# Kernel optimization log

Measured on AMD Instinct MI355X. Metric: run time of the kernel, lower is better.

## Reference

```python
import jax, jax.numpy as jnp
import numpy as np

START_ID = 1  # id of the start symbol in the vocabulary


def setup_inputs() -> dict:
    key = jax.random.key(0)
    ks = jax.random.split(key, 11)
    B, T, V, E, H, F = 64, 32, 10000, 300, 256, 4096
    s = 0.05
    return {
        "X": jax.random.normal(ks[0], (B, F), jnp.float32),
        "emb_table": jax.random.normal(ks[1], (V, E), jnp.float32),
        "fc1_w": jax.random.normal(ks[2], (H, F), jnp.float32) * s,
        "fc1_b": jax.random.normal(ks[3], (H,), jnp.float32) * s,
        "w_ih": jax.random.normal(ks[4], (4 * H, H + E), jnp.float32) * s,
        "w_hh": jax.random.normal(ks[5], (4 * H, H), jnp.float32) * s,
        "b_ih": jax.random.normal(ks[6], (4 * H,), jnp.float32) * s,
        "b_hh": jax.random.normal(ks[7], (4 * H,), jnp.float32) * s,
        "fc2_w": jax.random.normal(ks[8], (V, H), jnp.float32) * s,
        "fc2_b": jax.random.normal(ks[9], (V,), jnp.float32) * s,
        "label": jax.random.randint(ks[10], (T, B), 0, V, jnp.int64),
        "max_sentence_len": T,
    }


def reference(X, emb_table, fc1_w, fc1_b, w_ih, w_hh, b_ih, b_hh, fc2_w, fc2_b,
              label, max_sentence_len):
    T = max_sentence_len
    B = X.shape[0]
    V, H = fc2_w.shape
    E = emb_table.shape[1]

    # fc1: project image features to hidden size
    Xp = X @ fc1_w.T + fc1_b  # [B, H]

    # word embedding input per step: step 1 uses start symbol,
    # step idx>=2 uses teacher-forced embedding of label[idx-1]
    start_emb = jnp.broadcast_to(emb_table[START_ID], (1, B, E))
    tf_emb = emb_table[label[1:T - 1]]          # [T-2, B, E]
    embeds = jnp.concatenate([start_emb, tf_emb], axis=0)  # [T-1, B, E]

    h0 = jnp.zeros((B, H), X.dtype)
    c0 = jnp.zeros((B, H), X.dtype)

    def step(carry, e):
        h, c = carry
        x = jnp.concatenate([Xp, e], axis=1)  # [B, H+E]
        gates = x @ w_ih.T + b_ih + h @ w_hh.T + b_hh  # [B, 4H]
        i, f, g, o = jnp.split(gates, 4, axis=1)
        i = jax.nn.sigmoid(i)
        f = jax.nn.sigmoid(f)
        g = jnp.tanh(g)
        o = jax.nn.sigmoid(o)
        c = f * c + i * g
        h = o * jnp.tanh(c)
        logp = jax.nn.log_softmax(h @ fc2_w.T + fc2_b, axis=-1)  # [B, V]
        return (h, c), logp

    _, probs = jax.lax.scan(step, (h0, c0), embeds)  # [T-1, B, V]

    # first timestep: one-hot of the start word (as in the torch code)
    start_onehot = jnp.zeros((1, B, V), X.dtype).at[:, :, START_ID].set(1.0)
    result = jnp.concatenate([start_onehot, probs], axis=0)  # [T, B, V]
    return jnp.transpose(result, (1, 0, 2))  # [B, T, V]
```

## Files before the change

### kernel.cpp

```cpp
#include <hip/hip_runtime.h>
#include <hip/hip_bf16.h>
#include <math.h>

#define B_   64
#define T_   32
#define S_   31
#define V_   10000
#define E_   300
#define H_   256
#define F_   4096
#define G4   1024
#define HE   556
#define MPAD 2048
#define NPAD 10112
#define START_ID 1
#define NBL  4

#define FP0 10112
#define FP1 (FP0 + 128)
#define FP2 (FP1 + 2500)
#define FP3 (FP2 + 512)
#define FP4 (FP3 + 300)

typedef __bf16 bf16x8 __attribute__((ext_vector_type(8)));
typedef float  f32x4  __attribute__((ext_vector_type(4)));

__device__ __forceinline__ float bf16bits_to_f(unsigned int u) {
    union { unsigned int i; float f; } c; c.i = u; return c.f;
}
__device__ __forceinline__ unsigned short f_to_bf16bits(float f) {
    union { float f; unsigned int i; } c; c.f = f;
    unsigned int r = c.i + 0x7fffu + ((c.i >> 16) & 1);
    return (unsigned short)(r >> 16);
}
__device__ __forceinline__ float sigm(float x) { return 1.f / (1.f + __expf(-x)); }
__device__ __forceinline__ float tanh_fast(float x) { return 1.f - 2.f / (__expf(2.f * x) + 1.f); }

__device__ __forceinline__ void pina(bf16x8 &v) {
    union { bf16x8 b; unsigned int u[4]; } x;
    x.b = v;
    asm volatile("" : "+a"(x.u[0]), "+a"(x.u[1]), "+a"(x.u[2]), "+a"(x.u[3]));
    v = x.b;
}

__global__ void k_front(const float* __restrict__ fc2_w,
                        __hip_bfloat16* __restrict__ fc2bf,
                        __hip_bfloat16* __restrict__ Hs,
                        const float* __restrict__ w_hh,
                        unsigned short* __restrict__ wpack,
                        float* __restrict__ out,
                        const float* __restrict__ X,
                        const float* __restrict__ fc1_w,
                        const float* __restrict__ fc1_b,
                        float* __restrict__ Xp_part,
                        const float* __restrict__ w_ih,
                        float* __restrict__ wie) {
    int bid = blockIdx.x, tid = threadIdx.x;
    if (bid < FP0) {
        size_t i = (size_t)bid * 256 + tid;
        float v = (i < (size_t)V_ * H_) ? fc2_w[i] : 0.f;
        fc2bf[i] = __float2bfloat16(v);
        if (i < (size_t)(MPAD - S_ * B_) * H_)
            Hs[(size_t)S_ * B_ * H_ + i] = __float2bfloat16(0.f);
    } else if (bid < FP1) {
        int t = (bid - FP0) * 256 + tid;
        int lane = t & 63, frag = t >> 6;
        int kf = frag & 7, nt = (frag >> 3) & 7, w = frag >> 6;
        int l16 = lane & 15, quad = lane >> 4;
        int j = (l16 & 3) * 256 + w * 32 + nt * 4 + (l16 >> 2);
        int k0 = kf * 32 + quad * 8;
        const float* src = w_hh + (size_t)j * H_ + k0;
        float4 a0 = *(const float4*)(src);
        float4 a1 = *(const float4*)(src + 4);
        unsigned short pk[8];
        pk[0] = f_to_bf16bits(a0.x); pk[1] = f_to_bf16bits(a0.y);
        pk[2] = f_to_bf16bits(a0.z); pk[3] = f_to_bf16bits(a0.w);
        pk[4] = f_to_bf16bits(a1.x); pk[5] = f_to_bf16bits(a1.y);
        pk[6] = f_to_bf16bits(a1.z); pk[7] = f_to_bf16bits(a1.w);
        uint4 st;
        st.x = (unsigned)pk[0] | ((unsigned)pk[1] << 16);
        st.y = (unsigned)pk[2] | ((unsigned)pk[3] << 16);
        st.z = (unsigned)pk[4] | ((unsigned)pk[5] << 16);
        st.w = (unsigned)pk[6] | ((unsigned)pk[7] << 16);
        *(uint4*)(wpack + (size_t)frag * 512 + lane * 8) = st;
    } else if (bid < FP2) {
        int i = (bid - FP1) * 256 + tid;
        if (i < B_ * V_) {
            int b = i / V_, v = i - b * V_;
            out[(size_t)b * T_ * V_ + v] = (v == START_ID) ? 1.f : 0.f;
        }
    } else if (bid < FP3) {
        __shared__ __align__(16) float xs[512];
        int r = bid - FP2;
        int b = r >> 3, q = r & 7;
        const float4* xrow = (const float4*)(X + (size_t)b * F_ + q * 512);
        if (tid < 128) ((float4*)xs)[tid] = xrow[tid];
        __syncthreads();
        int k = tid;
        const float4* w = (const float4*)(fc1_w + (size_t)k * F_ + q * 512);
        float acc = 0.f;
        #pragma unroll 8
        for (int f = 0; f < 128; ++f) {
            float4 wv = w[f];
            float4 xv = ((const float4*)xs)[f];
            acc += wv.x * xv.x + wv.y * xv.y + wv.z * xv.z + wv.w * xv.w;
        }
        if (q == 0) acc += fc1_b[k];
        Xp_part[((size_t)(q * 64 + b)) * 256 + k] = acc;
    } else if (bid < FP4) {
        int idx = (bid - FP3) * 256 + tid;
        int kk = idx >> 10, j = idx & 1023;
        float4 v = *(const float4*)(w_ih + (size_t)j * HE + H_ + kk * 4);
        ((float4*)wie)[(size_t)kk * 1024 + j] = v;
    }
}

__global__ void k_gconst(const float* __restrict__ Xp_part, const float* __restrict__ w_ih,
                         const float* __restrict__ b_ih, const float* __restrict__ b_hh,
                         float* __restrict__ gconst) {
    __shared__ __align__(16) float xs[H_];
    int b = blockIdx.x;
    float s = 0.f;
    #pragma unroll
    for (int q = 0; q < 8; ++q) s += Xp_part[((size_t)(q * 64 + b)) * 256 + threadIdx.x];
    xs[threadIdx.x] = s;
    __syncthreads();
    #pragma unroll
    for (int q = 0; q < 4; ++q) {
        int j = threadIdx.x + q * 256;
        const float* w = w_ih + (size_t)j * HE;
        float acc = 0.f;
        #pragma unroll 8
        for (int k = 0; k < H_ / 4; ++k) {
            float4 wv = *(const float4*)(w + k * 4);
            float4 xv = ((const float4*)xs)[k];
            acc += wv.x * xv.x + wv.y * xv.y + wv.z * xv.z + wv.w * xv.w;
        }
        gconst[b * G4 + j] = acc + b_ih[j] + b_hh[j];
    }
}

__global__ void k_ge(const float* __restrict__ emb, const int* __restrict__ label,
                     const float* __restrict__ wie, const float* __restrict__ gconst,
                     unsigned short* __restrict__ gfullT) {
    __shared__ __align__(16) float es[8][E_];
    int jt = blockIdx.x, bt = blockIdx.y, t = blockIdx.z;
    for (int i = threadIdx.x; i < 8 * E_; i += 256) {
        int b8 = i / E_, e = i - b8 * E_;
        int b = bt * 8 + b8;
        int idx = (t == 0) ? START_ID : label[t * B_ + b];
        es[b8][e] = emb[(size_t)idx * E_ + e];
    }
    __syncthreads();
    int j = jt * 256 + threadIdx.x;
    const float4* wp4 = (const float4*)wie + j;
    float acc[8] = {0.f, 0.f, 0.f, 0.f, 0.f, 0.f, 0.f, 0.f};
    for (int kk = 0; kk < E_ / 4; ++kk) {
        float4 wv = wp4[(size_t)kk * 1024];
        #pragma unroll
        for (int b8 = 0; b8 < 8; ++b8) {
            float4 ev = *(const float4*)(&es[b8][kk * 4]);
            acc[b8] += wv.x * ev.x + wv.y * ev.y + wv.z * ev.z + wv.w * ev.w;
        }
    }
    int u = threadIdx.x;
    int tile = u >> 2;
    int m = (u & 3) * 4 + jt;
    size_t base = ((((size_t)t * NBL + (bt >> 1)) * 64 + tile) * 16 + (bt & 1) * 8) * 16 + m;
    #pragma unroll
    for (int b8 = 0; b8 < 8; ++b8)
        gfullT[base + (size_t)b8 * 16] =
            f_to_bf16bits(acc[b8] + gconst[(bt * 8 + b8) * G4 + j]);
}

__global__ __launch_bounds__(512)
__attribute__((amdgpu_waves_per_eu(2, 2)))
void k_lstm(const unsigned short* __restrict__ gfullT,
            const unsigned short* __restrict__ wpack,
            __hip_bfloat16* __restrict__ Hs_) {
    unsigned short* Hs = (unsigned short*)Hs_;
    int bg = blockIdx.x;
    int tid = threadIdx.x;
    int w = tid >> 6, lane = tid & 63;
    int l16 = lane & 15, quad = lane >> 4;

    __shared__ __align__(16) unsigned short hs0[16 * 264];
    __shared__ __align__(16) unsigned short hs1[16 * 264];
    __shared__ __align__(16) unsigned short blds[8 * 16 * 64 * 8];

    const unsigned short* wpb = wpack + (size_t)(w * 8) * 8 * 512 + lane * 8;

    bf16x8 wr0[8], wr1[8], wr2[8], wr3[8];
    #pragma unroll
    for (int kf = 0; kf < 8; ++kf) {
        wr0[kf] = *(const bf16x8*)(wpb + (0 * 8 + kf) * 512);
        wr1[kf] = *(const bf16x8*)(wpb + (1 * 8 + kf) * 512);
        wr2[kf] = *(const bf16x8*)(wpb + (2 * 8 + kf) * 512);
        wr3[kf] = *(const bf16x8*)(wpb + (3 * 8 + kf) * 512);
    }
    #pragma unroll
    for (int kf = 0; kf < 8; ++kf) {
        pina(wr0[kf]); pina(wr1[kf]); pina(wr2[kf]); pina(wr3[kf]);
    }

    #pragma unroll
    for (int f2 = 0; f2 < 16; ++f2) {
        int nt = 4 + (f2 >> 3), kf = f2 & 7;
        bf16x8 v = *(const bf16x8*)(wpb + (nt * 8 + kf) * 512);
        *(bf16x8*)(blds + ((size_t)(w * 16 + f2) * 64 + lane) * 8) = v;
    }

    for (int i = tid; i < 16 * 264 / 8; i += 512)
        ((uint4*)hs0)[i] = make_uint4(0, 0, 0, 0);
    __syncthreads();

    float c[8] = {0.f, 0.f, 0.f, 0.f, 0.f, 0.f, 0.f, 0.f};
    const unsigned short* bl = blds + (size_t)(w * 16) * 512 + lane * 8;
    int orow = tid >> 5, ocol = tid & 31;

    for (int t = 0; t < S_; ++t) {
        unsigned short* hcur = (t & 1) ? hs1 : hs0;
        unsigned short* hnxt = (t & 1) ? hs0 : hs1;

        const unsigned short* hb = hcur + l16 * 264 + quad * 8;
        bf16x8 hf[8];
        #pragma unroll
        for (int kf = 0; kf < 8; ++kf) hf[kf] = *(const bf16x8*)(hb + kf * 32);

        if (t > 0) {
            uint4 wv = *(const uint4*)(hcur + orow * 264 + ocol * 8);
            *(uint4*)(Hs + ((size_t)((t - 1) * B_ + bg * 16 + orow)) * H_ + ocol * 8) = wv;
        }
        uint2 gf[8];
        const unsigned short* gtb = gfullT +
            ((((size_t)t * NBL + bg) * 64 + w * 8) * 256) + l16 * 16 + quad * 4;
        #pragma unroll
        for (int nt = 0; nt < 8; ++nt) gf[nt] = *(const uint2*)(gtb + nt * 256);
        bf16x8 s6[8];
        #pragma unroll
        for (int kf = 0; kf < 8; ++kf) s6[kf] = *(const bf16x8*)(wpb + (6 * 8 + kf) * 512);

#define DO_NT(nt, WSRC)                                                          \
        {                                                                        \
            f32x4 acc0 = {0.f, 0.f, 0.f, 0.f}, acc1 = {0.f, 0.f, 0.f, 0.f};      \
            _Pragma("unroll")                                                    \
            for (int kf = 0; kf < 8; kf += 2) {                                  \
                acc0 = __builtin_amdgcn_mfma_f32_16x16x32_bf16(WSRC[kf], hf[kf], \
                                                               acc0, 0, 0, 0);  \
                acc1 = __builtin_amdgcn_mfma_f32_16x16x32_bf16(WSRC[kf + 1],     \
                                                               hf[kf + 1],      \
                                                               acc1, 0, 0, 0);  \
            }                                                                    \
            float g0 = acc0[0] + acc1[0] + bf16bits_to_f(gf[nt].x << 16);        \
            float g1 = acc0[1] + acc1[1] + bf16bits_to_f(gf[nt].x & 0xffff0000u);\
            float g2 = acc0[2] + acc1[2] + bf16bits_to_f(gf[nt].y << 16);        \
            float g3 = acc0[3] + acc1[3] + bf16bits_to_f(gf[nt].y & 0xffff0000u);\
            float ig = sigm(g0);                                                 \
            float fg = sigm(g1);                                                 \
            float gg = tanh_fast(g2);                                            \
            float og = sigm(g3);                                                 \
            c[nt] = fg * c[nt] + ig * gg;                                        \
            float hv = og * tanh_fast(c[nt]);                                    \
            hnxt[l16 * 264 + w * 32 + (nt) * 4 + quad] = f_to_bf16bits(hv);      \
        }

        DO_NT(0, wr0)
        DO_NT(1, wr1)
        DO_NT(2, wr2)
        DO_NT(3, wr3)
        {
            bf16x8 w4[8];
            #pragma unroll
            for (int kf = 0; kf < 8; ++kf) w4[kf] = *(const bf16x8*)(bl + kf * 512);
            DO_NT(4, w4)
        }
        bf16x8 s7[8];
        #pragma unroll
        for (int kf = 0; kf < 8; ++kf) s7[kf] = *(const bf16x8*)(wpb + (7 * 8 + kf) * 512);
        {
            bf16x8 w5[8];
            #pragma unroll
            for (int kf = 0; kf < 8; ++kf) w5[kf] = *(const bf16x8*)(bl + (8 + kf) * 512);
            DO_NT(5, w5)
        }
        DO_NT(6, s6)
        DO_NT(7, s7)
#undef DO_NT
        __syncthreads();
    }
    {
        uint4 v = *(const uint4*)(hs1 + orow * 264 + ocol * 8);
        *(uint4*)(Hs + ((size_t)((S_ - 1) * B_ + bg * 16 + orow)) * H_ + ocol * 8) = v;
    }
}

__global__ __launch_bounds__(256) void k_gemm(const unsigned short* __restrict__ A,
                                              const unsigned short* __restrict__ Bw,
                                              const float* __restrict__ bias,
                                              float* __restrict__ out) {
    int nt = blockIdx.x, mt = blockIdx.y;
    int w = threadIdx.x >> 6, lane = threadIdx.x & 63;
    int l16 = lane & 15, quad = lane >> 4;
    int m0 = mt * 128 + (w >> 1) * 64;
    int n0 = nt * 128 + (w & 1) * 64;
    f32x4 acc[4][4] = {};
    const unsigned short* Ap = A + (size_t)(m0 + l16) * H_ + quad * 8;
    const unsigned short* Bp = Bw + (size_t)(n0 + l16) * H_ + quad * 8;
    #pragma unroll
    for (int k = 0; k < H_; k += 32) {
        bf16x8 a[4], bb[4];
        #pragma unroll
        for (int i = 0; i < 4; ++i) {
            a[i]  = *(const bf16x8*)(Ap + (size_t)i * 16 * H_ + k);
            bb[i] = *(const bf16x8*)(Bp + (size_t)i * 16 * H_ + k);
        }
        #pragma unroll
        for (int i = 0; i < 4; ++i)
            #pragma unroll
            for (int jn = 0; jn < 4; ++jn)
                acc[i][jn] = __builtin_amdgcn_mfma_f32_16x16x32_bf16(a[i], bb[jn], acc[i][jn], 0, 0, 0);
    }
    #pragma unroll
    for (int i = 0; i < 4; ++i) {
        #pragma unroll
        for (int jn = 0; jn < 4; ++jn) {
            #pragma unroll
            for (int r = 0; r < 4; ++r) {
                int m = m0 + i * 16 + quad * 4 + r;
                int n = n0 + jn * 16 + l16;
                if (m < S_ * B_ && n < V_) {
                    int t = m >> 6, b = m & 63;
                    out[((size_t)b * T_ + t + 1) * V_ + n] = acc[i][jn][r] + bias[n];
                }
            }
        }
    }
}

__global__ __launch_bounds__(256) void k_lsm(float* __restrict__ out) {
    __shared__ __align__(16) float rowbuf[V_];
    __shared__ float rmx[256], rsum[256];
    int m = blockIdx.x;
    int t = m >> 6, b = m & 63;
    float* row = out + ((size_t)b * T_ + t + 1) * V_;
    int tid = threadIdx.x;
    float mx = -1e30f, sum = 0.f;
    for (int v4 = tid; v4 < V_ / 4; v4 += 256) {
        float4 x = ((const float4*)row)[v4];
        ((float4*)rowbuf)[v4] = x;
        float m4 = fmaxf(fmaxf(x.x, x.y), fmaxf(x.z, x.w));
        if (m4 > mx) { sum *= __expf(mx - m4); mx = m4; }
        sum += __expf(x.x - mx) + __expf(x.y - mx) + __expf(x.z - mx) + __expf(x.w - mx);
    }
    rmx[tid] = mx; rsum[tid] = sum;
    __syncthreads();
    for (int s = 128; s > 0; s >>= 1) {
        if (tid < s) {
            float ma = rmx[tid], mb = rmx[tid + s];
            float sa = rsum[tid], sb = rsum[tid + s];
            float mm = fmaxf(ma, mb);
            rmx[tid] = mm;
            rsum[tid] = sa * __expf(ma - mm) + sb * __expf(mb - mm);
        }
        __syncthreads();
    }
    float lse = rmx[0] + logf(rsum[0]);
    for (int v4 = tid; v4 < V_ / 4; v4 += 256) {
        float4 x = ((const float4*)rowbuf)[v4];
        x.x -= lse; x.y -= lse; x.z -= lse; x.w -= lse;
        ((float4*)row)[v4] = x;
    }
}

extern "C" void kernel_launch(void* const* d_in, const int* in_sizes, int n_in,
                              void* d_out, int out_size, void* d_ws, size_t ws_size,
                              hipStream_t stream) {
    const float* X      = (const float*)d_in[0];
    const float* emb    = (const float*)d_in[1];
    const float* fc1_w  = (const float*)d_in[2];
    const float* fc1_b  = (const float*)d_in[3];
    const float* w_ih   = (const float*)d_in[4];
    const float* w_hh   = (const float*)d_in[5];
    const float* b_ih   = (const float*)d_in[6];
    const float* b_hh   = (const float*)d_in[7];
    const float* fc2_w  = (const float*)d_in[8];
    const float* fc2_b  = (const float*)d_in[9];
    const int*   label  = (const int*)d_in[10];
    float* out = (float*)d_out;

    char* ws = (char*)d_ws;
    float*          Xp_part = (float*)(ws);
    float*          gconst  = (float*)(ws + 524288);
    unsigned short* gfullT  = (unsigned short*)(ws + 786432);
    __hip_bfloat16* Hs      = (__hip_bfloat16*)(ws + 4849664);
    __hip_bfloat16* fc2bf   = (__hip_bfloat16*)(ws + 5898240);
    unsigned short* wpack   = (unsigned short*)(ws + 11075584);
    float*          wie     = (float*)(ws + 11599872);

    k_front <<<FP4, 256, 0, stream>>>(fc2_w, fc2bf, Hs, w_hh, wpack, out,
                                      X, fc1_w, fc1_b, Xp_part, w_ih, wie);
    k_gconst<<<B_, 256, 0, stream>>>(Xp_part, w_ih, b_ih, b_hh, gconst);
    k_ge    <<<dim3(4, 8, S_), 256, 0, stream>>>(emb, label, wie, gconst, gfullT);
    k_lstm  <<<NBL, 512, 0, stream>>>(gfullT, wpack, Hs);
    k_gemm  <<<dim3(NPAD / 128, MPAD / 128), 256, 0, stream>>>((const unsigned short*)Hs,
                                                              (const unsigned short*)fc2bf, fc2_b, out);
    k_lsm   <<<S_ * B_, 256, 0, stream>>>(out);
}
```

Baseline: 503.3 us.

## Fuse LSTM recurrence and fc2 GEMM into one kernel with progress flags

Merges the LSTM recurrence kernel and the output-projection GEMM into a single launch. Four blocks run the recurrence and publish per-timestep progress counters with release atomics. The remaining 252 blocks loop over 256x128 GEMM tiles, spin-waiting with acquire loads until the hidden states their tile needs are written. This lets the projection overlap the serial recurrence instead of waiting for it to finish. It also drops the AGPR pinning and waves_per_eu hint, and seeds the MFMA accumulator with the gate preactivation in a single chain instead of two partial accumulators. The risks are that the spin-waiting blocks compete with the LSTM blocks for resources, and that the longer single MFMA dependency chain adds latency to each recurrence step.

```diff
diff --git a/kernel.cpp b/kernel.cpp
--- a/kernel.cpp
+++ b/kernel.cpp
@@ -15,6 +15,8 @@
 #define NPAD 10112
 #define START_ID 1
 #define NBL  4
+#define NW   252
+#define NTIL (8 * 79)
 
 #define FP0 10112
 #define FP1 (FP0 + 128)
@@ -35,13 +37,6 @@
 }
 __device__ __forceinline__ float sigm(float x) { return 1.f / (1.f + __expf(-x)); }
 __device__ __forceinline__ float tanh_fast(float x) { return 1.f - 2.f / (__expf(2.f * x) + 1.f); }
-
-__device__ __forceinline__ void pina(bf16x8 &v) {
-    union { bf16x8 b; unsigned int u[4]; } x;
-    x.b = v;
-    asm volatile("" : "+a"(x.u[0]), "+a"(x.u[1]), "+a"(x.u[2]), "+a"(x.u[3]));
-    v = x.b;
-}
 
 __global__ void k_front(const float* __restrict__ fc2_w,
                         __hip_bfloat16* __restrict__ fc2bf,
@@ -54,7 +49,8 @@
                         const float* __restrict__ fc1_b,
                         float* __restrict__ Xp_part,
                         const float* __restrict__ w_ih,
-                        float* __restrict__ wie) {
+                        float* __restrict__ wie,
+                        unsigned int* __restrict__ prog) {
     int bid = blockIdx.x, tid = threadIdx.x;
     if (bid < FP0) {
         size_t i = (size_t)bid * 256 + tid;
@@ -62,6 +58,7 @@
         fc2bf[i] = __float2bfloat16(v);
         if (i < (size_t)(MPAD - S_ * B_) * H_)
             Hs[(size_t)S_ * B_ * H_ + i] = __float2bfloat16(0.f);
+        if (bid == 0 && tid < 32) prog[tid] = 0u;
     } else if (bid < FP1) {
         int t = (bid - FP0) * 256 + tid;
         int lane = t & 63, frag = t >> 6;
@@ -174,12 +171,14 @@
 }
 
 __global__ __launch_bounds__(512)
-__attribute__((amdgpu_waves_per_eu(2, 2)))
-void k_lstm(const unsigned short* __restrict__ gfullT,
+void k_back(const unsigned short* __restrict__ gfullT,
             const unsigned short* __restrict__ wpack,
-            __hip_bfloat16* __restrict__ Hs_) {
+            __hip_bfloat16* __restrict__ Hs_,
+            const unsigned short* __restrict__ fc2bf,
+            const float* __restrict__ fc2_b,
+            float* __restrict__ out,
+            unsigned int* __restrict__ prog) {
     unsigned short* Hs = (unsigned short*)Hs_;
-    int bg = blockIdx.x;
     int tid = threadIdx.x;
     int w = tid >> 6, lane = tid & 63;
     int l16 = lane & 15, quad = lane >> 4;
@@ -188,149 +187,155 @@
     __shared__ __align__(16) unsigned short hs1[16 * 264];
     __shared__ __align__(16) unsigned short blds[8 * 16 * 64 * 8];
 
-    const unsigned short* wpb = wpack + (size_t)(w * 8) * 8 * 512 + lane * 8;
-
-    bf16x8 wr0[8], wr1[8], wr2[8], wr3[8];
-    #pragma unroll
-    for (int kf = 0; kf < 8; ++kf) {
-        wr0[kf] = *(const bf16x8*)(wpb + (0 * 8 + kf) * 512);
-        wr1[kf] = *(const bf16x8*)(wpb + (1 * 8 + kf) * 512);
-        wr2[kf] = *(const bf16x8*)(wpb + (2 * 8 + kf) * 512);
-        wr3[kf] = *(const bf16x8*)(wpb + (3 * 8 + kf) * 512);
-    }
-    #pragma unroll
-    for (int kf = 0; kf < 8; ++kf) {
-        pina(wr0[kf]); pina(wr1[kf]); pina(wr2[kf]); pina(wr3[kf]);
-    }
-
-    #pragma unroll
-    for (int f2 = 0; f2 < 16; ++f2) {
-        int nt = 4 + (f2 >> 3), kf = f2 & 7;
-        bf16x8 v = *(const bf16x8*)(wpb + (nt * 8 + kf) * 512);
-        *(bf16x8*)(blds + ((size_t)(w * 16 + f2) * 64 + lane) * 8) = v;
-    }
-
-    for (int i = tid; i < 16 * 264 / 8; i += 512)
-        ((uint4*)hs0)[i] = make_uint4(0, 0, 0, 0);
-    __syncthreads();
-
-    float c[8] = {0.f, 0.f, 0.f, 0.f, 0.f, 0.f, 0.f, 0.f};
-    const unsigned short* bl = blds + (size_t)(w * 16) * 512 + lane * 8;
-    int orow = tid >> 5, ocol = tid & 31;
-
-    for (int t = 0; t < S_; ++t) {
-        unsigned short* hcur = (t & 1) ? hs1 : hs0;
-        unsigned short* hnxt = (t & 1) ? hs0 : hs1;
-
-        const unsigned short* hb = hcur + l16 * 264 + quad * 8;
-        bf16x8 hf[8];
+    if (blockIdx.x < NBL) {
+        int bg = blockIdx.x;
+        const unsigned short* wpb = wpack + (size_t)(w * 8) * 8 * 512 + lane * 8;
+
+        bf16x8 wr0[8], wr1[8], wr2[8], wr3[8];
         #pragma unroll
-        for (int kf = 0; kf < 8; ++kf) hf[kf] = *(const bf16x8*)(hb + kf * 32);
-
-        if (t > 0) {
-            uint4 wv = *(const uint4*)(hcur + orow * 264 + ocol * 8);
-            *(uint4*)(Hs + ((size_t)((t - 1) * B_ + bg * 16 + orow)) * H_ + ocol * 8) = wv;
-        }
-        uint2 gf[8];
-        const unsigned short* gtb = gfullT +
-            ((((size_t)t * NBL + bg) * 64 + w * 8) * 256) + l16 * 16 + quad * 4;
+        for (int kf = 0; kf < 8; ++kf) {
+            wr0[kf] = *(const bf16x8*)(wpb + (0 * 8 + kf) * 512);
+            wr1[kf] = *(const bf16x8*)(wpb + (1 * 8 + kf) * 512);
+            wr2[kf] = *(const bf16x8*)(wpb + (2 * 8 + kf) * 512);
+            wr3[kf] = *(const bf16x8*)(wpb + (3 * 8 + kf) * 512);
+        }
         #pragma unroll
-        for (int nt = 0; nt < 8; ++nt) gf[nt] = *(const uint2*)(gtb + nt * 256);
-        bf16x8 s6[8];
-        #pragma unroll
-        for (int kf = 0; kf < 8; ++kf) s6[kf] = *(const bf16x8*)(wpb + (6 * 8 + kf) * 512);
-
-#define DO_NT(nt, WSRC)                                                          \
-        {                                                                        \
-            f32x4 acc0 = {0.f, 0.f, 0.f, 0.f}, acc1 = {0.f, 0.f, 0.f, 0.f};      \
-            _Pragma("unroll")                                                    \
-            for (int kf = 0; kf < 8; kf += 2) {                                  \
-                acc0 = __builtin_amdgcn_mfma_f32_16x16x32_bf16(WSRC[kf], hf[kf], \
-                                                               acc0, 0, 0, 0);  \
-                acc1 = __builtin_amdgcn_mfma_f32_16x16x32_bf16(WSRC[kf + 1],     \
-                                                               hf[kf + 1],      \
-                                                               acc1, 0, 0, 0);  \
-            }                                                                    \
-            float g0 = acc0[0] + acc1[0] + bf16bits_to_f(gf[nt].x << 16);        \
-            float g1 = acc0[1] + acc1[1] + bf16bits_to_f(gf[nt].x & 0xffff0000u);\
-            float g2 = acc0[2] + acc1[2] + bf16bits_to_f(gf[nt].y << 16);        \
-            float g3 = acc0[3] + acc1[3] + bf16bits_to_f(gf[nt].y & 0xffff0000u);\
-            float ig = sigm(g0);                                                 \
-            float fg = sigm(g1);                                                 \
-            float gg = tanh_fast(g2);                                            \
-            float og = sigm(g3);                                                 \
-            c[nt] = fg * c[nt] + ig * gg;                                        \
-            float hv = og * tanh_fast(c[nt]);                                    \
-            hnxt[l16 * 264 + w * 32 + (nt) * 4 + quad] = f_to_bf16bits(hv);      \
-        }
-
-        DO_NT(0, wr0)
-        DO_NT(1, wr1)
-        DO_NT(2, wr2)
-        DO_NT(3, wr3)
+        for (int f2 = 0; f2 < 16; ++f2) {
+            int nt = 4 + (f2 >> 3), kf = f2 & 7;
+            bf16x8 v = *(const bf16x8*)(wpb + (nt * 8 + kf) * 512);
+            *(bf16x8*)(blds + ((size_t)(w * 16 + f2) * 64 + lane) * 8) = v;
+        }
+        for (int i = tid; i < 16 * 264 / 8; i += 512)
+            ((uint4*)hs0)[i] = make_uint4(0, 0, 0, 0);
+        __syncthreads();
+
+        float c[8] = {0.f, 0.f, 0.f, 0.f, 0.f, 0.f, 0.f, 0.f};
+        const unsigned short* bl = blds + (size_t)(w * 16) * 512 + lane * 8;
+        int orow = tid >> 5, ocol = tid & 31;
+
+        for (int t = 0; t < S_; ++t) {
+            unsigned short* hcur = (t & 1) ? hs1 : hs0;
+            unsigned short* hnxt = (t & 1) ? hs0 : hs1;
+
+            const unsigned short* hb = hcur + l16 * 264 + quad * 8;
+            bf16x8 hf[8];
+            #pragma unroll
+            for (int kf = 0; kf < 8; ++kf) hf[kf] = *(const bf16x8*)(hb + kf * 32);
+
+            if (t > 0) {
+                uint4 wv = *(const uint4*)(hcur + orow * 264 + ocol * 8);
+                *(uint4*)(Hs + ((size_t)((t - 1) * B_ + bg * 16 + orow)) * H_ + ocol * 8) = wv;
+            }
+            uint2 gf[8];
+            const unsigned short* gtb = gfullT +
+                ((((size_t)t * NBL + bg) * 64 + w * 8) * 256) + l16 * 16 + quad * 4;
+            #pragma unroll
+            for (int nt = 0; nt < 8; ++nt) gf[nt] = *(const uint2*)(gtb + nt * 256);
+            bf16x8 s6[8];
+            #pragma unroll
+            for (int kf = 0; kf < 8; ++kf) s6[kf] = *(const bf16x8*)(wpb + (6 * 8 + kf) * 512);
+
+#define DO_NT(nt, WSRC)                                                         \
+            {                                                                   \
+                f32x4 acc;                                                      \
+                acc[0] = bf16bits_to_f(gf[nt].x << 16);                         \
+                acc[1] = bf16bits_to_f(gf[nt].x & 0xffff0000u);                 \
+                acc[2] = bf16bits_to_f(gf[nt].y << 16);                         \
+                acc[3] = bf16bits_to_f(gf[nt].y & 0xffff0000u);                 \
+                _Pragma("unroll")                                               \
+                for (int kf = 0; kf < 8; ++kf)                                  \
+                    acc = __builtin_amdgcn_mfma_f32_16x16x32_bf16(WSRC[kf],     \
+                                                  hf[kf], acc, 0, 0, 0);       \
+                float ig = sigm(acc[0]);                                        \
+                float fg = sigm(acc[1]);                                        \
+                float gg = tanh_fast(acc[2]);                                   \
+                float og = sigm(acc[3]);                                        \
+                c[nt] = fg * c[nt] + ig * gg;                                   \
+                float hv = og * tanh_fast(c[nt]);                               \
+                hnxt[l16 * 264 + w * 32 + (nt) * 4 + quad] = f_to_bf16bits(hv); \
+            }
+
+            DO_NT(0, wr0)
+            DO_NT(1, wr1)
+            DO_NT(2, wr2)
+            DO_NT(3, wr3)
+            {
+                bf16x8 w4[8];
+                #pragma unroll
+                for (int kf = 0; kf < 8; ++kf) w4[kf] = *(const bf16x8*)(bl + kf * 512);
+                DO_NT(4, w4)
+            }
+            bf16x8 s7[8];
+            #pragma unroll
+            for (int kf = 0; kf < 8; ++kf) s7[kf] = *(const bf16x8*)(wpb + (7 * 8 + kf) * 512);
+            {
+                bf16x8 w5[8];
+                #pragma unroll
+                for (int kf = 0; kf < 8; ++kf) w5[kf] = *(const bf16x8*)(bl + (8 + kf) * 512);
+                DO_NT(5, w5)
+            }
+            DO_NT(6, s6)
+            DO_NT(7, s7)
+#undef DO_NT
+            __syncthreads();
+            if (tid == 0 && t > 0)
+                __hip_atomic_fetch_add(&prog[t - 1], 1u, __ATOMIC_RELEASE,
+                                       __HIP_MEMORY_SCOPE_AGENT);
+        }
         {
-            bf16x8 w4[8];
-            #pragma unroll
-            for (int kf = 0; kf < 8; ++kf) w4[kf] = *(const bf16x8*)(bl + kf * 512);
-            DO_NT(4, w4)
-        }
-        bf16x8 s7[8];
-        #pragma unroll
-        for (int kf = 0; kf < 8; ++kf) s7[kf] = *(const bf16x8*)(wpb + (7 * 8 + kf) * 512);
-        {
-            bf16x8 w5[8];
-            #pragma unroll
-            for (int kf = 0; kf < 8; ++kf) w5[kf] = *(const bf16x8*)(bl + (8 + kf) * 512);
-            DO_NT(5, w5)
-        }
-        DO_NT(6, s6)
-        DO_NT(7, s7)
-#undef DO_NT
+            uint4 v = *(const uint4*)(hs1 + orow * 264 + ocol * 8);
+            *(uint4*)(Hs + ((size_t)((S_ - 1) * B_ + bg * 16 + orow)) * H_ + ocol * 8) = v;
+        }
         __syncthreads();
-    }
-    {
-        uint4 v = *(const uint4*)(hs1 + orow * 264 + ocol * 8);
-        *(uint4*)(Hs + ((size_t)((S_ - 1) * B_ + bg * 16 + orow)) * H_ + ocol * 8) = v;
-    }
-}
-
-__global__ __launch_bounds__(256) void k_gemm(const unsigned short* __restrict__ A,
-                                              const unsigned short* __restrict__ Bw,
-                                              const float* __restrict__ bias,
-                                              float* __restrict__ out) {
-    int nt = blockIdx.x, mt = blockIdx.y;
-    int w = threadIdx.x >> 6, lane = threadIdx.x & 63;
-    int l16 = lane & 15, quad = lane >> 4;
-    int m0 = mt * 128 + (w >> 1) * 64;
-    int n0 = nt * 128 + (w & 1) * 64;
-    f32x4 acc[4][4] = {};
-    const unsigned short* Ap = A + (size_t)(m0 + l16) * H_ + quad * 8;
-    const unsigned short* Bp = Bw + (size_t)(n0 + l16) * H_ + quad * 8;
-    #pragma unroll
-    for (int k = 0; k < H_; k += 32) {
-        bf16x8 a[4], bb[4];
-        #pragma unroll
-        for (int i = 0; i < 4; ++i) {
-            a[i]  = *(const bf16x8*)(Ap + (size_t)i * 16 * H_ + k);
-            bb[i] = *(const bf16x8*)(Bp + (size_t)i * 16 * H_ + k);
-        }
-        #pragma unroll
-        for (int i = 0; i < 4; ++i)
-            #pragma unroll
-            for (int jn = 0; jn < 4; ++jn)
-                acc[i][jn] = __builtin_amdgcn_mfma_f32_16x16x32_bf16(a[i], bb[jn], acc[i][jn], 0, 0, 0);
-    }
-    #pragma unroll
-    for (int i = 0; i < 4; ++i) {
-        #pragma unroll
-        for (int jn = 0; jn < 4; ++jn) {
-            #pragma unroll
-            for (int r = 0; r < 4; ++r) {
-                int m = m0 + i * 16 + quad * 4 + r;
-                int n = n0 + jn * 16 + l16;
-                if (m < S_ * B_ && n < V_) {
-                    int t = m >> 6, b = m & 63;
-                    out[((size_t)b * T_ + t + 1) * V_ + n] = acc[i][jn][r] + bias[n];
+        if (tid == 0)
+            __hip_atomic_fetch_add(&prog[S_ - 1], 1u, __ATOMIC_RELEASE,
+                                   __HIP_MEMORY_SCOPE_AGENT);
+    } else {
+        int wid = blockIdx.x - NBL;
+        for (int idx = wid; idx < NTIL; idx += NW) {
+            int mt = idx / 79, nt = idx - mt * 79;
+            int t_hi = mt * 4 + 3; if (t_hi > S_ - 1) t_hi = S_ - 1;
+            if (tid == 0) {
+                while (__hip_atomic_load(&prog[t_hi], __ATOMIC_ACQUIRE,
+                                         __HIP_MEMORY_SCOPE_AGENT) < (unsigned)NBL)
+                    __builtin_amdgcn_s_sleep(8);
+            }
+            __syncthreads();
+
+            int m0 = mt * 256 + (w & 3) * 64;
+            int n0 = nt * 128 + (w >> 2) * 64;
+            f32x4 acc[4][4] = {};
+            const unsigned short* Ap = Hs + (size_t)(m0 + l16) * H_ + quad * 8;
+            const unsigned short* Bp = fc2bf + (size_t)(n0 + l16) * H_ + quad * 8;
+            #pragma unroll
+            for (int k = 0; k < H_; k += 32) {
+                bf16x8 a[4], bb[4];
+                #pragma unroll
+                for (int i = 0; i < 4; ++i) {
+                    a[i]  = *(const bf16x8*)(Ap + (size_t)i * 16 * H_ + k);
+                    bb[i] = *(const bf16x8*)(Bp + (size_t)i * 16 * H_ + k);
+                }
+                #pragma unroll
+                for (int i = 0; i < 4; ++i)
+                    #pragma unroll
+                    for (int jn = 0; jn < 4; ++jn)
+                        acc[i][jn] = __builtin_amdgcn_mfma_f32_16x16x32_bf16(
+                            a[i], bb[jn], acc[i][jn], 0, 0, 0);
+            }
+            #pragma unroll
+            for (int i = 0; i < 4; ++i) {
+                #pragma unroll
+                for (int jn = 0; jn < 4; ++jn) {
+                    #pragma unroll
+                    for (int r = 0; r < 4; ++r) {
+                        int m = m0 + i * 16 + quad * 4 + r;
+                        int n = n0 + jn * 16 + l16;
+                        if (m < S_ * B_ && n < V_) {
+                            int t = m >> 6, b = m & 63;
+                            out[((size_t)b * T_ + t + 1) * V_ + n] =
+                                acc[i][jn][r] + fc2_b[n];
+                        }
+                    }
                 }
             }
         }
@@ -396,13 +401,13 @@
     __hip_bfloat16* fc2bf   = (__hip_bfloat16*)(ws + 5898240);
     unsigned short* wpack   = (unsigned short*)(ws + 11075584);
     float*          wie     = (float*)(ws + 11599872);
+    unsigned int*   prog    = (unsigned int*)(ws + 12828672);
 
     k_front <<<FP4, 256, 0, stream>>>(fc2_w, fc2bf, Hs, w_hh, wpack, out,
-                                      X, fc1_w, fc1_b, Xp_part, w_ih, wie);
+                                      X, fc1_w, fc1_b, Xp_part, w_ih, wie, prog);
     k_gconst<<<B_, 256, 0, stream>>>(Xp_part, w_ih, b_ih, b_hh, gconst);
     k_ge    <<<dim3(4, 8, S_), 256, 0, stream>>>(emb, label, wie, gconst, gfullT);
-    k_lstm  <<<NBL, 512, 0, stream>>>(gfullT, wpack, Hs);
-    k_gemm  <<<dim3(NPAD / 128, MPAD / 128), 256, 0, stream>>>((const unsigned short*)Hs,
-                                                              (const unsigned short*)fc2bf, fc2_b, out);
+    k_back  <<<NBL + NW, 512, 0, stream>>>(gfullT, wpack, Hs,
+                                           (const unsigned short*)fc2bf, fc2_b, out, prog);
     k_lsm   <<<S_ * B_, 256, 0, stream>>>(out);
 }
```

Result: slower. 717.4 us (+42.6%).
